# Performance work log

Measured on AMD Instinct MI355X. Metric: run time of the kernel, lower is better.

## Reference

```python
import jax, jax.numpy as jnp
import numpy as np
import math

HIDDEN = 2048
N_HEADS = 16
HEAD_DIM = HIDDEN // N_HEADS
BASE = 10000.0


def setup_inputs() -> dict:
    key = jax.random.key(0)
    ks = jax.random.split(key, 8)
    s = 1.0 / math.sqrt(HIDDEN)
    inp = {
        "hidden_states": jax.random.normal(ks[0], (2, 2048, HIDDEN), dtype=jnp.float32),
        "Wq": jax.random.normal(ks[1], (HIDDEN, HIDDEN), dtype=jnp.float32) * s,
        "bq": jax.random.normal(ks[2], (HIDDEN,), dtype=jnp.float32) * s,
        "Wk": jax.random.normal(ks[3], (HIDDEN, HIDDEN), dtype=jnp.float32) * s,
        "bk": jax.random.normal(ks[4], (HIDDEN,), dtype=jnp.float32) * s,
        "Wv": jax.random.normal(ks[5], (HIDDEN, HIDDEN), dtype=jnp.float32) * s,
        "bv": jax.random.normal(ks[6], (HIDDEN,), dtype=jnp.float32) * s,
        "Wo": jax.random.normal(ks[7], (HIDDEN, HIDDEN), dtype=jnp.float32) * s,
    }
    return inp


def _rotate_half(x):
    x1, x2 = x[..., : x.shape[-1] // 2], x[..., x.shape[-1] // 2 :]
    return jnp.concatenate((-x2, x1), axis=-1)


def _rope_cos_sin(seq_len, dtype):
    inv_freq = 1.0 / (BASE ** (jnp.arange(0, HEAD_DIM, 2, dtype=jnp.float32) / HEAD_DIM))
    t = jnp.arange(seq_len, dtype=jnp.float32)
    freqs = jnp.einsum("i,j->ij", t, inv_freq)  # [S, head_dim/2]
    emb = jnp.concatenate((freqs, freqs), axis=-1)  # [S, head_dim]
    return jnp.cos(emb).astype(dtype), jnp.sin(emb).astype(dtype)


def reference(hidden_states, Wq, bq, Wk, bk, Wv, bv, Wo):
    B, S, _ = hidden_states.shape
    q = hidden_states @ Wq + bq
    k = hidden_states @ Wk + bk
    v = hidden_states @ Wv + bv
    # [B, H, S, D]
    q = q.reshape(B, S, N_HEADS, HEAD_DIM).transpose(0, 2, 1, 3)
    k = k.reshape(B, S, N_HEADS, HEAD_DIM).transpose(0, 2, 1, 3)
    v = v.reshape(B, S, N_HEADS, HEAD_DIM).transpose(0, 2, 1, 3)
    cos, sin = _rope_cos_sin(S, q.dtype)  # [S, D]
    cos = cos[None, None]
    sin = sin[None, None]
    q = q * cos + _rotate_half(q) * sin
    k = k * cos + _rotate_half(k) * sin
    scale = 1.0 / math.sqrt(HEAD_DIM)
    scores = jnp.einsum("bhqd,bhkd->bhqk", q, k) * scale
    attn = jax.nn.softmax(scores, axis=-1)
    out = jnp.einsum("bhqk,bhkd->bhqd", attn, v)
    out = out.transpose(0, 2, 1, 3).reshape(B, S, HIDDEN)
    return out @ Wo
```

## Files before the change

kernel.cpp:

```cpp
#include <hip/hip_runtime.h>

#define HID 2048
#define SEQ 2048
#define HD 128
#define QKN 6144

typedef float f32x4 __attribute__((ext_vector_type(4)));
typedef short s16x8 __attribute__((ext_vector_type(8)));
typedef __bf16 bf16x8 __attribute__((ext_vector_type(8)));

static __device__ __forceinline__ unsigned short f2bf(float x) {
    unsigned u = __float_as_uint(x);
    u = u + 0x7FFFu + ((u >> 16) & 1u);
    return (unsigned short)(u >> 16);
}
static __device__ __forceinline__ float bf2f(unsigned short h) {
    return __uint_as_float(((unsigned)h) << 16);
}
static __device__ __forceinline__ bf16x8 as_bf(s16x8 v) {
    union { s16x8 s; bf16x8 b; } u; u.s = v; return u.b;
}
static __device__ __forceinline__ bf16x8 ld_bf8(const unsigned short* p) {
    return as_bf(*(const s16x8*)p);
}
static __device__ __forceinline__ void gload_lds16(const void* g, void* l) {
    __builtin_amdgcn_global_load_lds(
        (const __attribute__((address_space(1))) void*)g,
        (__attribute__((address_space(3))) void*)l,
        16, 0, 0);
}

__global__ __launch_bounds__(256) void fill_f32(
    float* __restrict__ out, float v, int n)
{
    int i = blockIdx.x * 256 + threadIdx.x;
    if (i < n) out[i] = v;
}

__global__ __launch_bounds__(256) void convert_f32_bf16(
    const float* __restrict__ in, unsigned short* __restrict__ out)
{
    long i = ((long)blockIdx.x * 256 + threadIdx.x) * 8;
    f32x4 a = *(const f32x4*)&in[i];
    f32x4 b = *(const f32x4*)&in[i + 4];
    s16x8 o;
#pragma unroll
    for (int e = 0; e < 4; ++e) {
        o[e]     = (short)f2bf(a[e]);
        o[e + 4] = (short)f2bf(b[e]);
    }
    *(s16x8*)&out[i] = o;
}

__global__ __launch_bounds__(256) void transpose_w(
    const float* __restrict__ W, unsigned short* __restrict__ Wt)
{
    __shared__ float t[32][33];
    int k0 = blockIdx.x * 32, n0 = blockIdx.y * 32;
    int tx = threadIdx.x & 31, ty = threadIdx.x >> 5;
#pragma unroll
    for (int r = ty; r < 32; r += 8)
        t[r][tx] = W[(long)(k0 + r) * HID + n0 + tx];
    __syncthreads();
#pragma unroll
    for (int r = ty; r < 32; r += 8)
        Wt[(long)(n0 + r) * HID + k0 + tx] = f2bf(t[tx][r]);
}

template<int NF, bool F32OUT>
__global__ __launch_bounds__(512, 2) void gemm_8phase(
    const unsigned short* __restrict__ A,
    const unsigned short* __restrict__ Bt,
    const float* __restrict__ bq, const float* __restrict__ bk,
    const float* __restrict__ bv,
    unsigned short* __restrict__ Cb, float* __restrict__ Cf,
    int K, int ldc, int nbn, int sm, int sn, int hasBias)
{
    constexpr int BUFE = 16384 + NF * 4096;
    __shared__ unsigned short lds[2 * BUFE];
    const int tid = threadIdx.x;
    const int wid = tid >> 6, lane = tid & 63;
    const int l16 = lane & 15, l4 = lane >> 4;
    const int wm = wid >> 2, wn = wid & 3;

    const int bid = blockIdx.x;
    const int xcd = bid & 7, idx = bid >> 3;
    const int ncn = nbn / sn;
    const int cm = xcd / ncn, cn = xcd % ncn;
    const int lm = idx / sn,  ln = idx % sn;
    const long bm = (long)(cm * sm + lm) * 256;
    const long bn = (long)(cn * sn + ln) * (NF * 64);

    const int NT = K >> 6;
    const long strideB = (long)K * 2;
    const int srow = tid >> 3;
    const int scb  = ((tid & 7) * 16) ^ ((srow & 7) << 4);

    auto stageA = [&](int t, int c) {
        unsigned short* base = &lds[(t & 1) * BUFE];
        const int row = c * 64 + srow;
        const char* src = (const char*)A + (bm + row) * strideB + (long)t * 128 + scb;
        gload_lds16(src, base + (c * 64 + wid * 8) * 64);
    };
    auto stageB = [&](int t, int c) {
        unsigned short* base = &lds[(t & 1) * BUFE + 16384];
        const int row = c * 64 + srow;
        const char* src = (const char*)Bt + (bn + row) * strideB + (long)t * 128 + scb;
        gload_lds16(src, base + (c * 64 + wid * 8) * 64);
    };

    f32x4 acc[8][NF];
#pragma unroll
    for (int i = 0; i < 8; ++i)
#pragma unroll
        for (int j = 0; j < NF; ++j) acc[i][j] = f32x4{0.f, 0.f, 0.f, 0.f};

    auto compute = [&](const unsigned short* Ab, const unsigned short* Bb) {
        bf16x8 bfr[NF][2];
#pragma unroll
        for (int j = 0; j < NF; ++j) {
            const int row = wn * (NF * 16) + j * 16 + l16;
            const char* rb = (const char*)Bb + row * 128;
#pragma unroll
            for (int kk = 0; kk < 2; ++kk)
                bfr[j][kk] = as_bf(*(const s16x8*)(rb + ((kk * 64 + l4 * 16) ^ ((l16 & 7) << 4))));
        }
#pragma unroll
        for (int half = 0; half < 2; ++half) {
            bf16x8 af[4][2];
#pragma unroll
            for (int i = 0; i < 4; ++i) {
                const int row = wm * 128 + (half * 4 + i) * 16 + l16;
                const char* rb = (const char*)Ab + row * 128;
#pragma unroll
                for (int kk = 0; kk < 2; ++kk)
                    af[i][kk] = as_bf(*(const s16x8*)(rb + ((kk * 64 + l4 * 16) ^ ((l16 & 7) << 4))));
            }
            __builtin_amdgcn_s_setprio(1);
#pragma unroll
            for (int kk = 0; kk < 2; ++kk)
#pragma unroll
                for (int i = 0; i < 4; ++i)
#pragma unroll
                    for (int j = 0; j < NF; ++j)
                        acc[half * 4 + i][j] = __builtin_amdgcn_mfma_f32_16x16x32_bf16(
                            af[i][kk], bfr[j][kk], acc[half * 4 + i][j], 0, 0, 0);
            __builtin_amdgcn_s_setprio(0);
        }
    };

#pragma unroll
    for (int c = 0; c < 4; ++c) stageA(0, c);
#pragma unroll
    for (int c = 0; c < NF; ++c) stageB(0, c);

    for (int t = 0; t < NT - 1; ++t) {
        const unsigned short* Ab = &lds[(t & 1) * BUFE];
        const unsigned short* Bb = Ab + 16384;
#pragma unroll
        for (int c = 0; c < 4; ++c) stageA(t + 1, c);
#pragma unroll
        for (int c = 0; c < NF; ++c) stageB(t + 1, c);
        __builtin_amdgcn_sched_barrier(0);
        if constexpr (NF == 3) asm volatile("s_waitcnt vmcnt(7)" ::: "memory");
        else                   asm volatile("s_waitcnt vmcnt(6)" ::: "memory");
        __builtin_amdgcn_s_barrier();
        __builtin_amdgcn_sched_barrier(0);
        compute(Ab, Bb);
        __builtin_amdgcn_s_barrier();
    }
    {
        const unsigned short* Ab = &lds[((NT - 1) & 1) * BUFE];
        const unsigned short* Bb = Ab + 16384;
        asm volatile("s_waitcnt vmcnt(0)" ::: "memory");
        __builtin_amdgcn_s_barrier();
        __builtin_amdgcn_sched_barrier(0);
        compute(Ab, Bb);
    }

#pragma unroll
    for (int nf = 0; nf < NF; ++nf) {
        const long n = bn + wn * (NF * 16) + nf * 16 + l16;
        float bvv = 0.f;
        if (hasBias)
            bvv = (n < HID) ? bq[n] : ((n < 2 * HID) ? bk[n - HID] : bv[n - 2 * HID]);
#pragma unroll
        for (int mf = 0; mf < 8; ++mf) {
#pragma unroll
            for (int r = 0; r < 4; ++r) {
                const long m = bm + wm * 128 + mf * 16 + l4 * 4 + r;
                float v = acc[mf][nf][r] + bvv;
                if (F32OUT) Cf[m * (long)ldc + n] = v;
                else        Cb[m * (long)ldc + n] = f2bf(v);
            }
        }
    }
}

__global__ __launch_bounds__(256) void rope_kernel(unsigned short* __restrict__ qkv)
{
    int t = blockIdx.x * 256 + threadIdx.x;
    int j8 = t & 7;
    int h  = (t >> 3) & 15;
    int qk = (t >> 7) & 1;
    int row = t >> 8;
    int s = row & (SEQ - 1);
    unsigned short* p = &qkv[(long)row * QKN + qk * HID + h * HD + j8 * 8];
    s16x8 lo = *(const s16x8*)p;
    s16x8 hi = *(const s16x8*)(p + 64);
    float qscale = qk ? 1.0f : 0.08838834764831845f;
    s16x8 olo, ohi;
#pragma unroll
    for (int e = 0; e < 8; ++e) {
        int j = j8 * 8 + e;
        float inv = exp2f(-(float)j * 0.20762050593046f);
        float sn, cs;
        sincosf((float)s * inv, &sn, &cs);
        float x1 = bf2f((unsigned short)lo[e]);
        float x2 = bf2f((unsigned short)hi[e]);
        olo[e] = (short)f2bf((x1 * cs - x2 * sn) * qscale);
        ohi[e] = (short)f2bf((x2 * cs + x1 * sn) * qscale);
    }
    *(s16x8*)p = olo;
    *(s16x8*)(p + 64) = ohi;
}

__global__ __launch_bounds__(256) void v_transpose(
    const unsigned short* __restrict__ qkv, unsigned short* __restrict__ vt)
{
    __shared__ unsigned short t[32][33];
    int bh = blockIdx.z;
    int b = bh >> 4, h = bh & 15;
    int s0 = blockIdx.x * 32, d0 = blockIdx.y * 32;
    int tx = threadIdx.x & 31, ty = threadIdx.x >> 5;
#pragma unroll
    for (int r = ty; r < 32; r += 8)
        t[r][tx] = qkv[(long)(b * SEQ + s0 + r) * QKN + 2 * HID + h * HD + d0 + tx];
    __syncthreads();
#pragma unroll
    for (int r = ty; r < 32; r += 8)
        vt[((long)bh * HD + d0 + r) * SEQ + s0 + tx] = t[tx][r];
}

__global__ __launch_bounds__(512) void attn_kernel(
    const unsigned short* __restrict__ qkv,
    const unsigned short* __restrict__ vt,
    unsigned short* __restrict__ attnout)
{
    __shared__ unsigned short Ks[2][64 * 128];
    __shared__ unsigned short Vs[2][128 * 64];

    const int tid = threadIdx.x, wid = tid >> 6, lane = tid & 63;
    const int l16 = lane & 15, l4 = lane >> 4;
    const int bid = blockIdx.x;
    const int xcd = bid & 7, idx = bid >> 3;
    const int bh = xcd * 4 + (idx >> 4);
    const int qt = idx & 15;
    const int b = bh >> 4, h = bh & 15;
    const long rowbase = (long)b * SEQ;

    const unsigned short* Kg = &qkv[rowbase * QKN + HID + h * HD];
    const unsigned short* Vg = &vt[(long)bh * HD * SEQ];

    auto stage = [&](int buf, int kv0) {
#pragma unroll
        for (int i = 0; i < 2; ++i) {
            int c = wid * 2 + i;
            int kr = c * 4 + l4;
            int kcb = (l16 * 16) ^ ((kr & 7) << 4);
            gload_lds16((const char*)(Kg + (long)(kv0 + kr) * QKN) + kcb, &Ks[buf][c * 512]);
            int vr = c * 8 + (lane >> 3);
            int vcb = ((lane & 7) * 16) ^ ((vr & 7) << 4);
            gload_lds16((const char*)(Vg + (long)vr * SEQ + kv0) + vcb, &Vs[buf][c * 512]);
        }
    };

    bf16x8 qf[4];
    {
        const long qrow = rowbase + qt * 128 + wid * 16 + l16;
        const unsigned short* qp = &qkv[qrow * QKN + h * HD];
#pragma unroll
        for (int kc = 0; kc < 4; ++kc) qf[kc] = ld_bf8(qp + kc * 32 + l4 * 8);
    }

    f32x4 o[8];
#pragma unroll
    for (int nb = 0; nb < 8; ++nb) o[nb] = f32x4{0.f, 0.f, 0.f, 0.f};
    float mrun = -3.0e38f, lrun = 0.f;

    const int srcA = ((l4 & 1) * 2) * 16 + l16;
    const int srcB = srcA + 16;
    const bool sel = (l4 >> 1) != 0;

    stage(0, 0);
    __syncthreads();

    for (int t = 0; t < SEQ / 64; ++t) {
        const int cur = t & 1;
        if (t < SEQ / 64 - 1) stage(cur ^ 1, (t + 1) * 64);
        __builtin_amdgcn_sched_barrier(0);

        const unsigned short* Kc = &Ks[cur][0];
        const unsigned short* Vc = &Vs[cur][0];

        f32x4 sc[4];
#pragma unroll
        for (int nf = 0; nf < 4; ++nf) sc[nf] = f32x4{0.f, 0.f, 0.f, 0.f};
#pragma unroll
        for (int kc = 0; kc < 4; ++kc) {
#pragma unroll
            for (int nf = 0; nf < 4; ++nf) {
                int row = nf * 16 + l16;
                int cb = (kc * 64 + l4 * 16) ^ ((row & 7) << 4);
                bf16x8 kf = as_bf(*(const s16x8*)((const char*)Kc + row * 256 + cb));
                sc[nf] = __builtin_amdgcn_mfma_f32_16x16x32_bf16(kf, qf[kc], sc[nf], 0, 0, 0);
            }
        }

        float tmax = sc[0][0];
#pragma unroll
        for (int nf = 0; nf < 4; ++nf)
#pragma unroll
            for (int r = 0; r < 4; ++r) tmax = fmaxf(tmax, sc[nf][r]);
        tmax = fmaxf(tmax, __shfl_xor(tmax, 16, 64));
        tmax = fmaxf(tmax, __shfl_xor(tmax, 32, 64));

        if (!__all(tmax - mrun <= 8.0f)) {
            float mn = fmaxf(mrun, tmax);
            float sc_ = __expf(mrun - mn);
            mrun = mn;
            lrun *= sc_;
            float s_[4];
#pragma unroll
            for (int r = 0; r < 4; ++r) s_[r] = __shfl(sc_, l4 * 4 + r, 64);
#pragma unroll
            for (int nb = 0; nb < 8; ++nb)
#pragma unroll
                for (int r = 0; r < 4; ++r) o[nb][r] *= s_[r];
        }

        unsigned pk[4][2];
        float sum = 0.f;
#pragma unroll
        for (int nf = 0; nf < 4; ++nf) {
            float p0 = __expf(sc[nf][0] - mrun);
            float p1 = __expf(sc[nf][1] - mrun);
            float p2 = __expf(sc[nf][2] - mrun);
            float p3 = __expf(sc[nf][3] - mrun);
            sum += (p0 + p1) + (p2 + p3);
            union { __bf16 b[2]; unsigned u; } w0, w1;
            w0.b[0] = (__bf16)p0; w0.b[1] = (__bf16)p1;
            w1.b[0] = (__bf16)p2; w1.b[1] = (__bf16)p3;
            pk[nf][0] = w0.u; pk[nf][1] = w1.u;
        }
        sum += __shfl_xor(sum, 16, 64);
        sum += __shfl_xor(sum, 32, 64);
        lrun += sum;

        union { unsigned u[4]; bf16x8 v; } pa0, pa1;
#pragma unroll
        for (int w = 0; w < 2; ++w) {
            unsigned a0 = __shfl(pk[0][w], srcA, 64);
            unsigned a1 = __shfl(pk[1][w], srcA, 64);
            unsigned b0 = __shfl(pk[0][w], srcB, 64);
            unsigned b1 = __shfl(pk[1][w], srcB, 64);
            pa0.u[w]     = sel ? a1 : a0;
            pa0.u[2 + w] = sel ? b1 : b0;
            unsigned c0 = __shfl(pk[2][w], srcA, 64);
            unsigned c1 = __shfl(pk[3][w], srcA, 64);
            unsigned d0 = __shfl(pk[2][w], srcB, 64);
            unsigned d1 = __shfl(pk[3][w], srcB, 64);
            pa1.u[w]     = sel ? c1 : c0;
            pa1.u[2 + w] = sel ? d1 : d0;
        }

#pragma unroll
        for (int kc = 0; kc < 2; ++kc) {
            bf16x8 pav = kc ? pa1.v : pa0.v;
#pragma unroll
            for (int nb = 0; nb < 8; ++nb) {
                int vrow = nb * 16 + l16;
                int vcb = (kc * 64 + l4 * 16) ^ ((vrow & 7) << 4);
                bf16x8 vb = as_bf(*(const s16x8*)((const char*)Vc + vrow * 128 + vcb));
                o[nb] = __builtin_amdgcn_mfma_f32_16x16x32_bf16(pav, vb, o[nb], 0, 0, 0);
            }
        }
        __syncthreads();
    }

    float linv = 1.f / lrun;
    float li[4];
#pragma unroll
    for (int r = 0; r < 4; ++r) li[r] = __shfl(linv, l4 * 4 + r, 64);
#pragma unroll
    for (int r = 0; r < 4; ++r) {
        long m = rowbase + qt * 128 + wid * 16 + l4 * 4 + r;
#pragma unroll
        for (int nb = 0; nb < 8; ++nb)
            attnout[m * HID + h * HD + nb * 16 + l16] = f2bf(o[nb][r] * li[r]);
    }
}

extern "C" void kernel_launch(void* const* d_in, const int* in_sizes, int n_in,
                              void* d_out, int out_size, void* d_ws, size_t ws_size,
                              hipStream_t stream)
{
    const float* hs = (const float*)d_in[0];
    const float* Wq = (const float*)d_in[1];
    const float* bq = (const float*)d_in[2];
    const float* Wk = (const float*)d_in[3];
    const float* bk = (const float*)d_in[4];
    const float* Wv = (const float*)d_in[5];
    const float* bv = (const float*)d_in[6];
    const float* Wo = (const float*)d_in[7];
    float* out = (float*)d_out;

    bool shapes_ok =
        (n_in == 8) && (out_size == 8388608) &&
        in_sizes[0] == 8388608 && in_sizes[1] == 4194304 && in_sizes[2] == 2048 &&
        in_sizes[3] == 4194304 && in_sizes[4] == 2048 && in_sizes[5] == 4194304 &&
        in_sizes[6] == 2048 && in_sizes[7] == 4194304;
    if (!shapes_ok || ws_size < 117440512ull) {
        fill_f32<<<32768, 256, 0, stream>>>(out, shapes_ok ? 1000.f : 0.f, out_size);
        return;
    }

    char* ws = (char*)d_ws;
    unsigned short* hsB     = (unsigned short*)(ws);
    unsigned short* qkvB    = (unsigned short*)(ws + 16777216);
    unsigned short* wqkvT   = (unsigned short*)(ws + 67108864);
    unsigned short* vtB     = (unsigned short*)(ws + 92274688);
    unsigned short* woT     = (unsigned short*)(ws + 109051904);
    unsigned short* attnout = hsB;

    convert_f32_bf16<<<4096, 256, 0, stream>>>(hs, hsB);
    dim3 tg(64, 64);
    transpose_w<<<tg, 256, 0, stream>>>(Wq, wqkvT);
    transpose_w<<<tg, 256, 0, stream>>>(Wk, wqkvT + 2048 * 2048);
    transpose_w<<<tg, 256, 0, stream>>>(Wv, wqkvT + 2 * 2048 * 2048);
    transpose_w<<<tg, 256, 0, stream>>>(Wo, woT);

    gemm_8phase<3, false><<<dim3(512), 512, 0, stream>>>(
        hsB, wqkvT, bq, bk, bv, qkvB, nullptr, 2048, QKN, 32, 8, 8, 1);
    rope_kernel<<<4096, 256, 0, stream>>>(qkvB);
    v_transpose<<<dim3(64, 4, 32), 256, 0, stream>>>(qkvB, vtB);
    attn_kernel<<<dim3(512), 512, 0, stream>>>(qkvB, vtB, attnout);
    gemm_8phase<2, true><<<dim3(256), 512, 0, stream>>>(
        attnout, woT, nullptr, nullptr, nullptr, nullptr, out, 2048, HID, 16, 4, 8, 0);
}
```

Before: 312.6 us.

## Process two 16-row query tiles per wave in attention kernel with 256 threads

Each wave of the attention kernel now handles 32 query rows as two independent 16-row tiles, so every K and V fragment read from LDS feeds two MFMAs. The block shrinks from 8 to 4 waves and each wave stages twice as many K/V chunks. The aim is to halve LDS read traffic per MFMA and give each wave more independent MFMA work. In exchange each wave roughly doubles its accumulator and softmax register use, which may lower occupancy, and there are fewer waves per block to hide latency.

```diff
diff --git a/kernel.cpp b/kernel.cpp
--- a/kernel.cpp
+++ b/kernel.cpp
@@ -242,7 +242,7 @@
         vt[((long)bh * HD + d0 + r) * SEQ + s0 + tx] = t[tx][r];
 }
 
-__global__ __launch_bounds__(512) void attn_kernel(
+__global__ __launch_bounds__(256) void attn_kernel(
     const unsigned short* __restrict__ qkv,
     const unsigned short* __restrict__ vt,
     unsigned short* __restrict__ attnout)
@@ -264,8 +264,8 @@
 
     auto stage = [&](int buf, int kv0) {
 #pragma unroll
-        for (int i = 0; i < 2; ++i) {
-            int c = wid * 2 + i;
+        for (int i = 0; i < 4; ++i) {
+            int c = wid * 4 + i;
             int kr = c * 4 + l4;
             int kcb = (l16 * 16) ^ ((kr & 7) << 4);
             gload_lds16((const char*)(Kg + (long)(kv0 + kr) * QKN) + kcb, &Ks[buf][c * 512]);
@@ -275,18 +275,23 @@
         }
     };
 
-    bf16x8 qf[4];
+    bf16x8 qf0[4], qf1[4];
     {
-        const long qrow = rowbase + qt * 128 + wid * 16 + l16;
-        const unsigned short* qp = &qkv[qrow * QKN + h * HD];
-#pragma unroll
-        for (int kc = 0; kc < 4; ++kc) qf[kc] = ld_bf8(qp + kc * 32 + l4 * 8);
-    }
-
-    f32x4 o[8];
-#pragma unroll
-    for (int nb = 0; nb < 8; ++nb) o[nb] = f32x4{0.f, 0.f, 0.f, 0.f};
-    float mrun = -3.0e38f, lrun = 0.f;
+        const long qr0 = rowbase + qt * 128 + wid * 32 + l16;
+        const unsigned short* qp0 = &qkv[qr0 * QKN + h * HD];
+        const unsigned short* qp1 = qp0 + 16 * QKN;
+#pragma unroll
+        for (int kc = 0; kc < 4; ++kc) {
+            qf0[kc] = ld_bf8(qp0 + kc * 32 + l4 * 8);
+            qf1[kc] = ld_bf8(qp1 + kc * 32 + l4 * 8);
+        }
+    }
+
+    f32x4 o0[8], o1[8];
+#pragma unroll
+    for (int nb = 0; nb < 8; ++nb) { o0[nb] = f32x4{0.f,0.f,0.f,0.f}; o1[nb] = f32x4{0.f,0.f,0.f,0.f}; }
+    float mrun0 = -3.0e38f, lrun0 = 0.f;
+    float mrun1 = -3.0e38f, lrun1 = 0.f;
 
     const int srcA = ((l4 & 1) * 2) * 16 + l16;
     const int srcB = srcA + 16;
@@ -303,9 +308,9 @@
         const unsigned short* Kc = &Ks[cur][0];
         const unsigned short* Vc = &Vs[cur][0];
 
-        f32x4 sc[4];
-#pragma unroll
-        for (int nf = 0; nf < 4; ++nf) sc[nf] = f32x4{0.f, 0.f, 0.f, 0.f};
+        f32x4 sc0[4], sc1[4];
+#pragma unroll
+        for (int nf = 0; nf < 4; ++nf) { sc0[nf] = f32x4{0.f,0.f,0.f,0.f}; sc1[nf] = f32x4{0.f,0.f,0.f,0.f}; }
 #pragma unroll
         for (int kc = 0; kc < 4; ++kc) {
 #pragma unroll
@@ -313,91 +318,133 @@
                 int row = nf * 16 + l16;
                 int cb = (kc * 64 + l4 * 16) ^ ((row & 7) << 4);
                 bf16x8 kf = as_bf(*(const s16x8*)((const char*)Kc + row * 256 + cb));
-                sc[nf] = __builtin_amdgcn_mfma_f32_16x16x32_bf16(kf, qf[kc], sc[nf], 0, 0, 0);
-            }
-        }
-
-        float tmax = sc[0][0];
+                sc0[nf] = __builtin_amdgcn_mfma_f32_16x16x32_bf16(kf, qf0[kc], sc0[nf], 0, 0, 0);
+                sc1[nf] = __builtin_amdgcn_mfma_f32_16x16x32_bf16(kf, qf1[kc], sc1[nf], 0, 0, 0);
+            }
+        }
+
+        float tmax0 = sc0[0][0], tmax1 = sc1[0][0];
 #pragma unroll
         for (int nf = 0; nf < 4; ++nf)
 #pragma unroll
-            for (int r = 0; r < 4; ++r) tmax = fmaxf(tmax, sc[nf][r]);
-        tmax = fmaxf(tmax, __shfl_xor(tmax, 16, 64));
-        tmax = fmaxf(tmax, __shfl_xor(tmax, 32, 64));
-
-        if (!__all(tmax - mrun <= 8.0f)) {
-            float mn = fmaxf(mrun, tmax);
-            float sc_ = __expf(mrun - mn);
-            mrun = mn;
-            lrun *= sc_;
-            float s_[4];
-#pragma unroll
-            for (int r = 0; r < 4; ++r) s_[r] = __shfl(sc_, l4 * 4 + r, 64);
+            for (int r = 0; r < 4; ++r) {
+                tmax0 = fmaxf(tmax0, sc0[nf][r]);
+                tmax1 = fmaxf(tmax1, sc1[nf][r]);
+            }
+        tmax0 = fmaxf(tmax0, __shfl_xor(tmax0, 16, 64));
+        tmax0 = fmaxf(tmax0, __shfl_xor(tmax0, 32, 64));
+        tmax1 = fmaxf(tmax1, __shfl_xor(tmax1, 16, 64));
+        tmax1 = fmaxf(tmax1, __shfl_xor(tmax1, 32, 64));
+
+        float grow = fmaxf(tmax0 - mrun0, tmax1 - mrun1);
+        if (!__all(grow <= 8.0f)) {
+            float mn0 = fmaxf(mrun0, tmax0), mn1 = fmaxf(mrun1, tmax1);
+            float e0 = __expf(mrun0 - mn0), e1 = __expf(mrun1 - mn1);
+            mrun0 = mn0; mrun1 = mn1;
+            lrun0 *= e0;  lrun1 *= e1;
+            float s0_[4], s1_[4];
+#pragma unroll
+            for (int r = 0; r < 4; ++r) {
+                s0_[r] = __shfl(e0, l4 * 4 + r, 64);
+                s1_[r] = __shfl(e1, l4 * 4 + r, 64);
+            }
 #pragma unroll
             for (int nb = 0; nb < 8; ++nb)
 #pragma unroll
-                for (int r = 0; r < 4; ++r) o[nb][r] *= s_[r];
-        }
-
-        unsigned pk[4][2];
-        float sum = 0.f;
+                for (int r = 0; r < 4; ++r) { o0[nb][r] *= s0_[r]; o1[nb][r] *= s1_[r]; }
+        }
+
+        unsigned pk0[4][2], pk1[4][2];
+        float sum0 = 0.f, sum1 = 0.f;
 #pragma unroll
         for (int nf = 0; nf < 4; ++nf) {
-            float p0 = __expf(sc[nf][0] - mrun);
-            float p1 = __expf(sc[nf][1] - mrun);
-            float p2 = __expf(sc[nf][2] - mrun);
-            float p3 = __expf(sc[nf][3] - mrun);
-            sum += (p0 + p1) + (p2 + p3);
+            float a0 = __expf(sc0[nf][0] - mrun0), a1 = __expf(sc0[nf][1] - mrun0);
+            float a2 = __expf(sc0[nf][2] - mrun0), a3 = __expf(sc0[nf][3] - mrun0);
+            sum0 += (a0 + a1) + (a2 + a3);
             union { __bf16 b[2]; unsigned u; } w0, w1;
-            w0.b[0] = (__bf16)p0; w0.b[1] = (__bf16)p1;
-            w1.b[0] = (__bf16)p2; w1.b[1] = (__bf16)p3;
-            pk[nf][0] = w0.u; pk[nf][1] = w1.u;
-        }
-        sum += __shfl_xor(sum, 16, 64);
-        sum += __shfl_xor(sum, 32, 64);
-        lrun += sum;
-
-        union { unsigned u[4]; bf16x8 v; } pa0, pa1;
+            w0.b[0] = (__bf16)a0; w0.b[1] = (__bf16)a1;
+            w1.b[0] = (__bf16)a2; w1.b[1] = (__bf16)a3;
+            pk0[nf][0] = w0.u; pk0[nf][1] = w1.u;
+            float b0 = __expf(sc1[nf][0] - mrun1), b1 = __expf(sc1[nf][1] - mrun1);
+            float b2 = __expf(sc1[nf][2] - mrun1), b3 = __expf(sc1[nf][3] - mrun1);
+            sum1 += (b0 + b1) + (b2 + b3);
+            union { __bf16 b[2]; unsigned u; } x0, x1;
+            x0.b[0] = (__bf16)b0; x0.b[1] = (__bf16)b1;
+            x1.b[0] = (__bf16)b2; x1.b[1] = (__bf16)b3;
+            pk1[nf][0] = x0.u; pk1[nf][1] = x1.u;
+        }
+        sum0 += __shfl_xor(sum0, 16, 64);
+        sum0 += __shfl_xor(sum0, 32, 64);
+        sum1 += __shfl_xor(sum1, 16, 64);
+        sum1 += __shfl_xor(sum1, 32, 64);
+        lrun0 += sum0; lrun1 += sum1;
+
+        union { unsigned u[4]; bf16x8 v; } pa00, pa01, pa10, pa11;
 #pragma unroll
         for (int w = 0; w < 2; ++w) {
-            unsigned a0 = __shfl(pk[0][w], srcA, 64);
-            unsigned a1 = __shfl(pk[1][w], srcA, 64);
-            unsigned b0 = __shfl(pk[0][w], srcB, 64);
-            unsigned b1 = __shfl(pk[1][w], srcB, 64);
-            pa0.u[w]     = sel ? a1 : a0;
-            pa0.u[2 + w] = sel ? b1 : b0;
-            unsigned c0 = __shfl(pk[2][w], srcA, 64);
-            unsigned c1 = __shfl(pk[3][w], srcA, 64);
-            unsigned d0 = __shfl(pk[2][w], srcB, 64);
-            unsigned d1 = __shfl(pk[3][w], srcB, 64);
-            pa1.u[w]     = sel ? c1 : c0;
-            pa1.u[2 + w] = sel ? d1 : d0;
+            {
+                unsigned a0 = __shfl(pk0[0][w], srcA, 64);
+                unsigned a1 = __shfl(pk0[1][w], srcA, 64);
+                unsigned b0 = __shfl(pk0[0][w], srcB, 64);
+                unsigned b1 = __shfl(pk0[1][w], srcB, 64);
+                pa00.u[w]     = sel ? a1 : a0;
+                pa00.u[2 + w] = sel ? b1 : b0;
+                unsigned c0 = __shfl(pk0[2][w], srcA, 64);
+                unsigned c1 = __shfl(pk0[3][w], srcA, 64);
+                unsigned d0 = __shfl(pk0[2][w], srcB, 64);
+                unsigned d1 = __shfl(pk0[3][w], srcB, 64);
+                pa01.u[w]     = sel ? c1 : c0;
+                pa01.u[2 + w] = sel ? d1 : d0;
+            }
+            {
+                unsigned a0 = __shfl(pk1[0][w], srcA, 64);
+                unsigned a1 = __shfl(pk1[1][w], srcA, 64);
+                unsigned b0 = __shfl(pk1[0][w], srcB, 64);
+                unsigned b1 = __shfl(pk1[1][w], srcB, 64);
+                pa10.u[w]     = sel ? a1 : a0;
+                pa10.u[2 + w] = sel ? b1 : b0;
+                unsigned c0 = __shfl(pk1[2][w], srcA, 64);
+                unsigned c1 = __shfl(pk1[3][w], srcA, 64);
+                unsigned d0 = __shfl(pk1[2][w], srcB, 64);
+                unsigned d1 = __shfl(pk1[3][w], srcB, 64);
+                pa11.u[w]     = sel ? c1 : c0;
+                pa11.u[2 + w] = sel ? d1 : d0;
+            }
         }
 
 #pragma unroll
         for (int kc = 0; kc < 2; ++kc) {
-            bf16x8 pav = kc ? pa1.v : pa0.v;
+            bf16x8 pav0 = kc ? pa01.v : pa00.v;
+            bf16x8 pav1 = kc ? pa11.v : pa10.v;
 #pragma unroll
             for (int nb = 0; nb < 8; ++nb) {
                 int vrow = nb * 16 + l16;
                 int vcb = (kc * 64 + l4 * 16) ^ ((vrow & 7) << 4);
                 bf16x8 vb = as_bf(*(const s16x8*)((const char*)Vc + vrow * 128 + vcb));
-                o[nb] = __builtin_amdgcn_mfma_f32_16x16x32_bf16(pav, vb, o[nb], 0, 0, 0);
+                o0[nb] = __builtin_amdgcn_mfma_f32_16x16x32_bf16(pav0, vb, o0[nb], 0, 0, 0);
+                o1[nb] = __builtin_amdgcn_mfma_f32_16x16x32_bf16(pav1, vb, o1[nb], 0, 0, 0);
             }
         }
         __syncthreads();
     }
 
-    float linv = 1.f / lrun;
-    float li[4];
-#pragma unroll
-    for (int r = 0; r < 4; ++r) li[r] = __shfl(linv, l4 * 4 + r, 64);
+    float li0[4], li1[4];
+    {
+        float linv0 = 1.f / lrun0, linv1 = 1.f / lrun1;
+#pragma unroll
+        for (int r = 0; r < 4; ++r) {
+            li0[r] = __shfl(linv0, l4 * 4 + r, 64);
+            li1[r] = __shfl(linv1, l4 * 4 + r, 64);
+        }
+    }
 #pragma unroll
     for (int r = 0; r < 4; ++r) {
-        long m = rowbase + qt * 128 + wid * 16 + l4 * 4 + r;
-#pragma unroll
-        for (int nb = 0; nb < 8; ++nb)
-            attnout[m * HID + h * HD + nb * 16 + l16] = f2bf(o[nb][r] * li[r]);
+        long m0 = rowbase + qt * 128 + wid * 32 + l4 * 4 + r;
+#pragma unroll
+        for (int nb = 0; nb < 8; ++nb) {
+            attnout[m0 * HID + h * HD + nb * 16 + l16] = f2bf(o0[nb][r] * li0[r]);
+            attnout[(m0 + 16) * HID + h * HD + nb * 16 + l16] = f2bf(o1[nb][r] * li1[r]);
+        }
     }
 }
 
@@ -444,7 +491,7 @@
         hsB, wqkvT, bq, bk, bv, qkvB, nullptr, 2048, QKN, 32, 8, 8, 1);
     rope_kernel<<<4096, 256, 0, stream>>>(qkvB);
     v_transpose<<<dim3(64, 4, 32), 256, 0, stream>>>(qkvB, vtB);
-    attn_kernel<<<dim3(512), 512, 0, stream>>>(qkvB, vtB, attnout);
+    attn_kernel<<<dim3(512), 256, 0, stream>>>(qkvB, vtB, attnout);
     gemm_8phase<2, true><<<dim3(256), 512, 0, stream>>>(
         attnout, woT, nullptr, nullptr, nullptr, nullptr, out, 2048, HID, 16, 4, 8, 0);
 }
```

New measurement: 363.4 us. 1.16x slower.
